# Optimization experiments

Measured on AMD Instinct MI355X. Metric: run time of the kernel, lower is better.

## Reference

```python
import jax, jax.numpy as jnp
import numpy as np
from jax import lax

# Surrogate spike: forward = Heaviside, backward = g / (1 + 5|x|)^2
@jax.custom_vjp
def spike_fn(x):
    return (x >= 0).astype(x.dtype)

def _spk_fwd(x):
    return spike_fn(x), x

def _spk_bwd(x, g):
    return (g / (1.0 + 5.0 * jnp.abs(x)) ** 2,)

spike_fn.defvjp(_spk_fwd, _spk_bwd)

BN_EPS = 1e-5

def _batchnorm(x, scale, bias, mean, var):
    # x: (B, C, T); eval-mode BN with running stats
    inv = scale / jnp.sqrt(var + BN_EPS)
    return x * inv[None, :, None] + (bias - mean * inv)[None, :, None]

def _conv1d(x, w, b, pad):
    y = lax.conv_general_dilated(x, w, (1,), [(pad, pad)],
                                 dimension_numbers=('NCH', 'OIH', 'NCH'))
    return y + b[None, :, None]

def setup_inputs() -> dict:
    key = jax.random.key(0)
    ks = jax.random.split(key, 12)
    B, T, EEG, GEO, TH, H, OUT = 4096, 320, 64, 18, 32, 16, 4
    inp = {
        'x_eeg': jax.random.normal(ks[0], (B, T, EEG), jnp.float32),
        'x_geo': jax.random.normal(ks[1], (B, T, GEO), jnp.float32),
        'conv1_w': jax.random.normal(ks[2], (TH, EEG, 5), jnp.float32) * 0.05,
        'conv1_b': jnp.zeros((TH,), jnp.float32),
        'bn1_s': jnp.ones((TH,), jnp.float32),
        'bn1_b': jnp.zeros((TH,), jnp.float32),
        'bn1_m': jnp.zeros((TH,), jnp.float32),
        'bn1_v': jnp.ones((TH,), jnp.float32),
        'conv2_w': jax.random.normal(ks[3], (H, TH, 3), jnp.float32) * 0.1,
        'conv2_b': jnp.zeros((H,), jnp.float32),
        'bn2_s': jnp.ones((H,), jnp.float32),
        'bn2_b': jnp.zeros((H,), jnp.float32),
        'bn2_m': jnp.zeros((H,), jnp.float32),
        'bn2_v': jnp.ones((H,), jnp.float32),
        'geo_w': jax.random.normal(ks[4], (H, GEO), jnp.float32) * 0.2,
        'geo_b': jnp.zeros((H,), jnp.float32),
        'gamma': jnp.full((H,), 0.5, jnp.float32),
        'fc1_w': jax.random.normal(ks[5], (64, 160), jnp.float32) * 0.08,
        'fc1_b': jnp.zeros((64,), jnp.float32),
        'fc2_w': jax.random.normal(ks[6], (OUT, 64), jnp.float32) * 0.12,
        'fc2_b': jnp.zeros((OUT,), jnp.float32),
    }
    return inp

def reference(x_eeg, x_geo, conv1_w, conv1_b, bn1_s, bn1_b, bn1_m, bn1_v,
              conv2_w, conv2_b, bn2_s, bn2_b, bn2_m, bn2_v,
              geo_w, geo_b, gamma, fc1_w, fc1_b, fc2_w, fc2_b):
    B, T, _ = x_eeg.shape
    theta_0, beta, tau_a, tau_m = 0.5, 1.8, 0.36, 0.8

    # EEG temporal encoder (eval mode: dropout = identity)
    h = x_eeg.transpose(0, 2, 1)  # (B, 64, T)
    h = jax.nn.relu(_batchnorm(_conv1d(h, conv1_w, conv1_b, 2), bn1_s, bn1_b, bn1_m, bn1_v))
    h = jax.nn.relu(_batchnorm(_conv1d(h, conv2_w, conv2_b, 1), bn2_s, bn2_b, bn2_m, bn2_v))
    eeg_encoded = h.transpose(0, 2, 1)  # (B, T, 16)

    geo_mod = jax.nn.sigmoid(jnp.einsum('bti,hi->bth', x_geo, geo_w) + geo_b)  # (B, T, 16)

    H = eeg_encoded.shape[-1]
    zeros = jnp.zeros((B, H), x_eeg.dtype)
    init = (zeros, zeros, zeros, zeros)  # mem_alif, eta, mem_li, prev_spk

    def step(carry, xs):
        mem_alif, eta, mem_li, prev_spk = carry
        cur_eeg, cur_geo = xs
        eta = tau_a * eta + (1.0 - tau_a) * prev_spk
        theta_t = theta_0 + beta * eta - gamma * cur_geo
        mem_alif = tau_m * mem_alif + cur_eeg
        spk = spike_fn(mem_alif - theta_t)
        mem_alif = mem_alif * (1.0 - spk)
        mem_li = 0.9 * mem_li + spk
        return (mem_alif, eta, mem_li, spk), mem_li

    xs = (eeg_encoded.transpose(1, 0, 2), geo_mod.transpose(1, 0, 2))  # (T, B, 16)
    _, pot = lax.scan(step, init, xs)  # (T, B, 16)

    pot = pot.transpose(1, 2, 0)                 # (B, 16, T)
    windows = pot.reshape(B, H, 10, 32)          # T = 320 = 10*32
    dp_feat = (windows[..., 16:].mean(-1) - windows[..., :16].mean(-1)).reshape(B, -1)  # (B, 160)

    out = jax.nn.relu(dp_feat @ fc1_w.T + fc1_b) @ fc2_w.T + fc2_b  # (B, 4)
    return out
```

## Files before the change

### kernel.cpp

```cpp
#include <hip/hip_runtime.h>
#include <math.h>

#define TB    4096
#define TSEQ  320
#define NEEG  64
#define NTH   32
#define NH    16
#define NGEO  18
#define TILE_T 64
#define NTILES 5
#define XROWS2 70
#define H1ROWS 66

typedef _Float16 f16x8 __attribute__((ext_vector_type(8)));
typedef _Float16 f16x2 __attribute__((ext_vector_type(2)));
typedef float f32x4 __attribute__((ext_vector_type(4)));
#define INV2048 4.8828125e-4f

#define OFF_W1F  0
#define OFF_W2F  10240
#define OFF_B1   11776
#define OFF_B2   11808
#define OFF_GWT  11824
#define OFF_FC1T 12112
#define OFF_FC2T 22352
#define OFF_ZP   22656
#define OFF_E    32768
#define SZ_EC    (TB*TSEQ*NH)
#define OFF_C    (OFF_E + SZ_EC)

__global__ void __launch_bounds__(256)
prep_kernel(const float* __restrict__ c1w, const float* __restrict__ c1b,
            const float* __restrict__ s1,  const float* __restrict__ bb1,
            const float* __restrict__ mm1, const float* __restrict__ vv1,
            const float* __restrict__ c2w, const float* __restrict__ c2b,
            const float* __restrict__ s2,  const float* __restrict__ bb2,
            const float* __restrict__ mm2, const float* __restrict__ vv2,
            const float* __restrict__ gw,  const float* __restrict__ fc1w,
            const float* __restrict__ fc2w, float* __restrict__ ws)
{
    const int tid = threadIdx.x;
    _Float16* w1fp = reinterpret_cast<_Float16*>(ws + OFF_W1F);
    _Float16* w2fp = reinterpret_cast<_Float16*>(ws + OFF_W2F);

    for (int d = tid; d < 10240; d += 256) {
        int j = d & 7, l = (d >> 3) & 63, nbk = d >> 9;
        int kk = nbk >> 1, nb = nbk & 1;
        int k = kk >> 1, i = (kk & 1) * 32 + ((l >> 4) * 8) + j;
        int c = nb * 16 + (l & 15);
        float inv = s1[c] / sqrtf(vv1[c] + 1e-5f);
        float wv = c1w[c * 320 + i * 5 + k] * inv;
        _Float16 hi = (_Float16)wv;
        _Float16 lo = (_Float16)((wv - (float)hi) * 2048.f);
        w1fp[((nbk * 2 + 0) * 64 + l) * 8 + j] = hi;
        w1fp[((nbk * 2 + 1) * 64 + l) * 8 + j] = lo;
    }
    for (int d = tid; d < 1536; d += 256) {
        int j = d & 7, l = (d >> 3) & 63, kk2 = d >> 9;
        int c = (l >> 4) * 8 + j;
        int o = l & 15;
        float inv = s2[o] / sqrtf(vv2[o] + 1e-5f);
        float wv = c2w[o * 96 + c * 3 + kk2] * inv;
        _Float16 hi = (_Float16)wv;
        _Float16 lo = (_Float16)((wv - (float)hi) * 2048.f);
        w2fp[((kk2 * 2 + 0) * 64 + l) * 8 + j] = hi;
        w2fp[((kk2 * 2 + 1) * 64 + l) * 8 + j] = lo;
    }
    if (tid < NTH) {
        float inv = s1[tid] / sqrtf(vv1[tid] + 1e-5f);
        ws[OFF_B1 + tid] = c1b[tid] * inv + bb1[tid] - mm1[tid] * inv;
    }
    if (tid < NH) {
        float inv = s2[tid] / sqrtf(vv2[tid] + 1e-5f);
        ws[OFF_B2 + tid] = c2b[tid] * inv + bb2[tid] - mm2[tid] * inv;
    }
    for (int d = tid; d < NGEO * NH; d += 256) {
        int i = d / NH, h = d - i * NH;
        ws[OFF_GWT + d] = gw[h * NGEO + i];
    }
    for (int d = tid; d < 160 * 64; d += 256) {
        int f = d / 64, o = d - f * 64;
        ws[OFF_FC1T + d] = fc1w[o * 160 + f];
    }
    if (tid < 256) {
        int j = tid / 4, o = tid - j * 4;
        ws[OFF_FC2T + tid] = fc2w[o * 64 + j];
    }
    if (tid < 64) ws[OFF_ZP + tid] = 0.f;
}

__global__ void __launch_bounds__(256, 2)
convm_kernel(const float* __restrict__ xeeg, const float* __restrict__ ws,
             float* __restrict__ E)
{
    __shared__ __align__(16) float xbuf[2][XROWS2 * 64];
    __shared__ __align__(16) _Float16 h1h[H1ROWS * 32];
    __shared__ __align__(16) _Float16 h1l[H1ROWS * 32];
    __shared__ float b1s[32], b2s[16];

    const int b = blockIdx.x, tid = threadIdx.x;
    const int l = tid & 63, w = tid >> 6;
    const int lrow = l & 15, lkg = l >> 4;
    const int nb = w >> 1, wsub = w & 1;

    const float* xb = xeeg + (size_t)b * TSEQ * NEEG;
    const float* zp = ws + OFF_ZP;

#define STAGE_DMA(buf, t0n) do {                                                     \
        for (int c_ = w; c_ < XROWS2; c_ += 4) {                                     \
            int tg_ = (t0n) - 3 + c_;                                                \
            const float* s_ = (tg_ >= 0 && tg_ < TSEQ)                               \
                              ? (xb + (size_t)tg_ * 64 + l) : zp;                    \
            __builtin_amdgcn_global_load_lds(                                        \
                (const __attribute__((address_space(1))) void*)s_,                   \
                (__attribute__((address_space(3))) void*)&xbuf[(buf)][c_ * 64],      \
                4, 0, 0);                                                            \
        }                                                                            \
    } while (0)

    f16x8 B1h[10], B1l[10], B2h[3], B2l[3];
    {
        const f16x8* wsrc = reinterpret_cast<const f16x8*>(ws + OFF_W1F);
        #pragma unroll
        for (int kk = 0; kk < 10; ++kk) {
            B1h[kk] = wsrc[((kk * 2 + nb) * 2 + 0) * 64 + l];
            B1l[kk] = wsrc[((kk * 2 + nb) * 2 + 1) * 64 + l];
        }
        const f16x8* wsrc2 = reinterpret_cast<const f16x8*>(ws + OFF_W2F);
        #pragma unroll
        for (int kk = 0; kk < 3; ++kk) {
            B2h[kk] = wsrc2[(kk * 2 + 0) * 64 + l];
            B2l[kk] = wsrc2[(kk * 2 + 1) * 64 + l];
        }
    }
    if (tid < 32) b1s[tid] = ws[OFF_B1 + tid];
    if (tid < 16) b2s[tid] = ws[OFF_B2 + tid];

    STAGE_DMA(0, 0);
    __syncthreads();

    for (int jt = 0; jt < NTILES; ++jt) {
        const int t0 = jt * TILE_T;
        const int cur = jt & 1;
        _Float16* xh = reinterpret_cast<_Float16*>(&xbuf[cur][0]);
        _Float16* xl = xh + XROWS2 * 64;

        float2 xr2[9];
        #pragma unroll
        for (int q = 0; q < 9; ++q) {
            int p = tid + q * 256;
            if (p < 2240) {
                int xr = p >> 5, ip = (p & 31) * 2;
                xr2[q] = *reinterpret_cast<const float2*>(&xbuf[cur][xr * 64 + ip]);
            }
        }
        __syncthreads();

        #pragma unroll
        for (int q = 0; q < 9; ++q) {
            int p = tid + q * 256;
            if (p < 2240) {
                int xr = p >> 5, ip = (p & 31) * 2;
                float f0 = xr2[q].x, f1 = xr2[q].y;
                _Float16 h0 = (_Float16)f0, h1v = (_Float16)f1;
                f16x2 vh = {h0, h1v};
                f16x2 vl = {(_Float16)((f0 - (float)h0) * 2048.f),
                            (_Float16)((f1 - (float)h1v) * 2048.f)};
                int idx = xr * 64 + (((ip >> 3) ^ (xr & 7)) << 3) + (ip & 7);
                *reinterpret_cast<f16x2*>(&xh[idx]) = vh;
                *reinterpret_cast<f16x2*>(&xl[idx]) = vl;
            }
        }
        __syncthreads();

        if (jt + 1 < NTILES) STAGE_DMA(cur ^ 1, (jt + 1) * TILE_T);
        __builtin_amdgcn_s_setprio(1);
        {
            const float bia = b1s[nb * 16 + lrow];
            #pragma unroll
            for (int pi = 0; pi < 3; ++pi) {
                if (pi == 2 && ((jt & 1) != wsub)) break;
                const int mb = (pi < 2) ? (wsub + pi * 2) : 4;
                const int mbase = mb * 16;
                int s = mbase + lrow; if (s > 65) s = 65;
                f32x4 aH = {0.f, 0.f, 0.f, 0.f};
                f32x4 aM = aH, aL = aH;
                #pragma unroll
                for (int kk = 0; kk < 10; ++kk) {
                    const int xr = s + (kk >> 1);
                    const int gx = (kk & 1) * 4 + lkg;
                    const int off = xr * 64 + ((gx ^ (xr & 7)) << 3);
                    f16x8 Ah = *reinterpret_cast<const f16x8*>(&xh[off]);
                    f16x8 Al = *reinterpret_cast<const f16x8*>(&xl[off]);
                    aH = __builtin_amdgcn_mfma_f32_16x16x32_f16(Ah, B1h[kk], aH, 0, 0, 0);
                    aM = __builtin_amdgcn_mfma_f32_16x16x32_f16(Ah, B1l[kk], aM, 0, 0, 0);
                    aL = __builtin_amdgcn_mfma_f32_16x16x32_f16(Al, B1h[kk], aL, 0, 0, 0);
                }
                #pragma unroll
                for (int r = 0; r < 4; ++r) {
                    int so = mbase + lkg * 4 + r;
                    if (so < 66) {
                        int tg = t0 - 1 + so;
                        bool v = (tg >= 0 && tg < TSEQ);
                        float val = v ? fmaxf(fmaf(aM[r] + aL[r], INV2048, aH[r]) + bia, 0.f) : 0.f;
                        int key = (so >> 1) & 3;
                        int g = (nb * 2 + (lrow >> 3)) ^ key;
                        int idx = so * 32 + (g << 3) + (lrow & 7);
                        _Float16 hh = (_Float16)val;
                        h1h[idx] = hh;
                        h1l[idx] = (_Float16)((val - (float)hh) * 2048.f);
                    }
                }
            }
        }
        __builtin_amdgcn_s_setprio(0);
        __syncthreads();

        {
            const int ub = w * 16;
            f32x4 aH = {0.f, 0.f, 0.f, 0.f};
            f32x4 aM = aH, aL = aH;
            __builtin_amdgcn_s_setprio(1);
            #pragma unroll
            for (int kk = 0; kk < 3; ++kk) {
                int srow = ub + lrow + kk;
                int off = srow * 32 + ((lkg ^ ((srow >> 1) & 3)) << 3);
                f16x8 Ah = *reinterpret_cast<const f16x8*>(&h1h[off]);
                f16x8 Al = *reinterpret_cast<const f16x8*>(&h1l[off]);
                aH = __builtin_amdgcn_mfma_f32_16x16x32_f16(Ah, B2h[kk], aH, 0, 0, 0);
                aM = __builtin_amdgcn_mfma_f32_16x16x32_f16(Ah, B2l[kk], aM, 0, 0, 0);
                aL = __builtin_amdgcn_mfma_f32_16x16x32_f16(Al, B2h[kk], aL, 0, 0, 0);
            }
            __builtin_amdgcn_s_setprio(0);
            const float bia = b2s[lrow];
            float4 ev;
            float* evp = reinterpret_cast<float*>(&ev);
            #pragma unroll
            for (int r = 0; r < 4; ++r)
                evp[r] = fmaxf(fmaf(aM[r] + aL[r], INV2048, aH[r]) + bia, 0.f);
            const int t4o = ((t0 + ub) >> 2) + lkg;
            float* ep = E + (((size_t)t4o * TB + b) * 16 + lrow) * 4;
            *reinterpret_cast<float4*>(ep) = ev;
        }
    }
#undef STAGE_DMA
}

__global__ void __launch_bounds__(256)
geo_kernel(const float* __restrict__ xgeo, const float* __restrict__ ws,
           const float* __restrict__ geo_b, const float* __restrict__ gamma,
           float* __restrict__ C)
{
    __shared__ float xgs[16][288];
    __shared__ float gws_l[NGEO * NH];
    __shared__ float gb_l[16], gam_l[16];

    const int tid = threadIdx.x;
    const int b0 = blockIdx.x * 16;
    const int s0 = blockIdx.y * 4;

    for (int p = tid; p < NGEO * NH; p += 256) gws_l[p] = ws[OFF_GWT + p];
    if (tid < 16) { gb_l[tid] = geo_b[tid]; gam_l[tid] = gamma[tid]; }
    {
        const float4* xg4 = reinterpret_cast<const float4*>(xgeo);
        for (int p = tid; p < 1152; p += 256) {
            int bb = p / 72, r = p - bb * 72;
            reinterpret_cast<float4*>(&xgs[bb][0])[r] =
                xg4[(size_t)(b0 + bb) * 1440 + (size_t)s0 * 18 + r];
        }
    }
    __syncthreads();

    const int h = tid & 15, bl = tid >> 4;
    #pragma unroll
    for (int k = 0; k < 4; ++k) {
        const int t4 = s0 + k;
        float4 cv;
        float* cvp = reinterpret_cast<float*>(&cv);
        #pragma unroll
        for (int tt = 0; tt < 4; ++tt) {
            float z = gb_l[h];
            const float* xr = &xgs[bl][(k * 4 + tt) * 18];
            #pragma unroll
            for (int ii = 0; ii < NGEO; ++ii)
                z = fmaf(xr[ii], gws_l[ii * 16 + h], z);
            cvp[tt] = gam_l[h] * (1.f / (1.f + expf(-z)));
        }
        float* cp = C + (((size_t)t4 * TB + (b0 + bl)) * 16 + h) * 4;
        *reinterpret_cast<float4*>(cp) = cv;
    }
}

__global__ void __launch_bounds__(256)
scanfc_kernel(const float* __restrict__ E, const float* __restrict__ C,
              const float* __restrict__ ws, const float* __restrict__ fc1_b,
              const float* __restrict__ fc2_b, float* __restrict__ out)
{
    __shared__ float dp_lds[16][160];
    __shared__ float mid[16][64];

    const int tid = threadIdx.x;
    const int h = tid & 15, bl = tid >> 4;
    const int b0 = blockIdx.x * 16;
    const int b = b0 + bl;

    const float4* e4 = reinterpret_cast<const float4*>(E);
    const float4* c4 = reinterpret_cast<const float4*>(C);
    const size_t slab = (size_t)TB * 16;
    const size_t idx = (size_t)b * 16 + h;

    float eta = 0.f, memv = 0.f, li = 0.f, ps = 0.f, accF = 0.f, accS = 0.f;

    float4 eA[4], cA[4], eB[4], cB[4];

#define LOADQ(EB, CB, lq) do {                                                   \
        if ((lq) < 20) {                                                         \
            _Pragma("unroll")                                                    \
            for (int j = 0; j < 4; ++j) {                                        \
                EB[j] = e4[(size_t)((lq) * 4 + j) * slab + idx];                 \
                CB[j] = c4[(size_t)((lq) * 4 + j) * slab + idx];                 \
            }                                                                    \
        }                                                                        \
    } while (0)

#define PROCQ(EB, CB, q) do {                                                    \
        _Pragma("unroll")                                                        \
        for (int j = 0; j < 4; ++j) {                                            \
            const int t4_ = (q) * 4 + j;                                         \
            const float* evp = reinterpret_cast<const float*>(&EB[j]);           \
            const float* cvp = reinterpret_cast<const float*>(&CB[j]);           \
            _Pragma("unroll")                                                    \
            for (int tt = 0; tt < 4; ++tt) {                                     \
                float e = evp[tt], c = cvp[tt];                                  \
                eta = 0.36f * eta + 0.64f * ps;                                  \
                float theta = 0.5f + 1.8f * eta - c;                             \
                memv = 0.8f * memv + e;                                          \
                float spk = (memv - theta >= 0.f) ? 1.f : 0.f;                   \
                memv *= (1.f - spk);                                             \
                li = 0.9f * li + spk;                                            \
                ps = spk;                                                        \
                int t = t4_ * 4 + tt;                                            \
                if (((t >> 4) & 1) == 0) accF += li; else accS += li;            \
            }                                                                    \
            if ((t4_ & 7) == 7) {                                                \
                dp_lds[bl][h * 10 + (t4_ >> 3)] = (accS - accF) * 0.0625f;       \
                accF = 0.f; accS = 0.f;                                          \
            }                                                                    \
        }                                                                        \
    } while (0)

    LOADQ(eA, cA, 0);
    for (int qp = 0; qp < 10; ++qp) {
        const int q0 = qp * 2, q1 = qp * 2 + 1;
        LOADQ(eB, cB, q1);
        PROCQ(eA, cA, q0);
        LOADQ(eA, cA, q1 + 1);
        PROCQ(eB, cB, q1);
    }
#undef LOADQ
#undef PROCQ
    __syncthreads();

    {
        const float* __restrict__ fc1t = ws + OFF_FC1T;
        #pragma unroll
        for (int k = 0; k < 4; ++k) {
            int id = tid + k * 256;
            int bb = id >> 6, o = id & 63;
            float z = fc1_b[o];
            for (int f = 0; f < 160; ++f)
                z = fmaf(dp_lds[bb][f], fc1t[f * 64 + o], z);
            mid[bb][o] = fmaxf(z, 0.f);
        }
    }
    __syncthreads();
    if (tid < 64) {
        const float* __restrict__ fc2t = ws + OFF_FC2T;
        int bb = tid >> 2, oo = tid & 3;
        float z = fc2_b[oo];
        #pragma unroll
        for (int jj = 0; jj < 64; ++jj)
            z = fmaf(mid[bb][jj], fc2t[jj * 4 + oo], z);
        out[(size_t)(b0 + bb) * 4 + oo] = z;
    }
}

extern "C" void kernel_launch(void* const* d_in, const int* in_sizes, int n_in,
                              void* d_out, int out_size, void* d_ws, size_t ws_size,
                              hipStream_t stream)
{
    const float* xeeg = (const float*)d_in[0];
    const float* xgeo = (const float*)d_in[1];
    const float* c1w  = (const float*)d_in[2];
    const float* c1b  = (const float*)d_in[3];
    const float* s1   = (const float*)d_in[4];
    const float* bb1  = (const float*)d_in[5];
    const float* mm1  = (const float*)d_in[6];
    const float* vv1  = (const float*)d_in[7];
    const float* c2w  = (const float*)d_in[8];
    const float* c2b  = (const float*)d_in[9];
    const float* s2   = (const float*)d_in[10];
    const float* bb2  = (const float*)d_in[11];
    const float* mm2  = (const float*)d_in[12];
    const float* vv2  = (const float*)d_in[13];
    const float* gw   = (const float*)d_in[14];
    const float* gb   = (const float*)d_in[15];
    const float* gam  = (const float*)d_in[16];
    const float* fc1w = (const float*)d_in[17];
    const float* fc1b = (const float*)d_in[18];
    const float* fc2w = (const float*)d_in[19];
    const float* fc2b = (const float*)d_in[20];
    float* ws   = (float*)d_ws;
    float* outp = (float*)d_out;

    hipLaunchKernelGGL(prep_kernel, dim3(1), dim3(256), 0, stream,
                       c1w, c1b, s1, bb1, mm1, vv1, c2w, c2b, s2, bb2, mm2, vv2,
                       gw, fc1w, fc2w, ws);

    float* E = ws + OFF_E;
    float* C = ws + OFF_C;
    hipLaunchKernelGGL(geo_kernel, dim3(TB / 16, TSEQ / 16), dim3(256), 0, stream,
                       xgeo, ws, gb, gam, C);
    hipLaunchKernelGGL(convm_kernel, dim3(TB), dim3(256), 0, stream,
                       xeeg, ws, E);
    hipLaunchKernelGGL(scanfc_kernel, dim3(TB / 16), dim3(256), 0, stream,
                       E, C, ws, fc1b, fc2b, outp);
}
```

Measured before the change: 300.7 us.

## Fuse geo modulation into scan kernel with double-buffered LDS staging of x_geo

Removes the separate geo_kernel and its intermediate C buffer (TB*T*16 floats written then read back). The scan kernel now stages x_geo tiles into a double-buffered shared array and computes the sigmoid-gated geo term inline per timestep. This saves the global round-trip of C and one kernel launch. In exchange it adds per-step FMA and exp work inside the serial scan and block-wide syncs, while the scan kernel only has 256 blocks.

```diff
diff --git a/kernel.cpp b/kernel.cpp
--- a/kernel.cpp
+++ b/kernel.cpp
@@ -27,7 +27,6 @@
 #define OFF_ZP   22656
 #define OFF_E    32768
 #define SZ_EC    (TB*TSEQ*NH)
-#define OFF_C    (OFF_E + SZ_EC)
 
 __global__ void __launch_bounds__(256)
 prep_kernel(const float* __restrict__ c1w, const float* __restrict__ c1b,
@@ -247,55 +246,14 @@
 }
 
 __global__ void __launch_bounds__(256)
-geo_kernel(const float* __restrict__ xgeo, const float* __restrict__ ws,
-           const float* __restrict__ geo_b, const float* __restrict__ gamma,
-           float* __restrict__ C)
+scanfc_kernel(const float* __restrict__ E, const float* __restrict__ xgeo,
+              const float* __restrict__ ws, const float* __restrict__ geo_b,
+              const float* __restrict__ gamma, const float* __restrict__ fc1_b,
+              const float* __restrict__ fc2_b, float* __restrict__ out)
 {
-    __shared__ float xgs[16][288];
+    __shared__ float xgs[2][16][288];
     __shared__ float gws_l[NGEO * NH];
     __shared__ float gb_l[16], gam_l[16];
-
-    const int tid = threadIdx.x;
-    const int b0 = blockIdx.x * 16;
-    const int s0 = blockIdx.y * 4;
-
-    for (int p = tid; p < NGEO * NH; p += 256) gws_l[p] = ws[OFF_GWT + p];
-    if (tid < 16) { gb_l[tid] = geo_b[tid]; gam_l[tid] = gamma[tid]; }
-    {
-        const float4* xg4 = reinterpret_cast<const float4*>(xgeo);
-        for (int p = tid; p < 1152; p += 256) {
-            int bb = p / 72, r = p - bb * 72;
-            reinterpret_cast<float4*>(&xgs[bb][0])[r] =
-                xg4[(size_t)(b0 + bb) * 1440 + (size_t)s0 * 18 + r];
-        }
-    }
-    __syncthreads();
-
-    const int h = tid & 15, bl = tid >> 4;
-    #pragma unroll
-    for (int k = 0; k < 4; ++k) {
-        const int t4 = s0 + k;
-        float4 cv;
-        float* cvp = reinterpret_cast<float*>(&cv);
-        #pragma unroll
-        for (int tt = 0; tt < 4; ++tt) {
-            float z = gb_l[h];
-            const float* xr = &xgs[bl][(k * 4 + tt) * 18];
-            #pragma unroll
-            for (int ii = 0; ii < NGEO; ++ii)
-                z = fmaf(xr[ii], gws_l[ii * 16 + h], z);
-            cvp[tt] = gam_l[h] * (1.f / (1.f + expf(-z)));
-        }
-        float* cp = C + (((size_t)t4 * TB + (b0 + bl)) * 16 + h) * 4;
-        *reinterpret_cast<float4*>(cp) = cv;
-    }
-}
-
-__global__ void __launch_bounds__(256)
-scanfc_kernel(const float* __restrict__ E, const float* __restrict__ C,
-              const float* __restrict__ ws, const float* __restrict__ fc1_b,
-              const float* __restrict__ fc2_b, float* __restrict__ out)
-{
     __shared__ float dp_lds[16][160];
     __shared__ float mid[16][64];
 
@@ -304,34 +262,47 @@
     const int b0 = blockIdx.x * 16;
     const int b = b0 + bl;
 
-    const float4* e4 = reinterpret_cast<const float4*>(E);
-    const float4* c4 = reinterpret_cast<const float4*>(C);
+    const float4* e4  = reinterpret_cast<const float4*>(E);
+    const float4* xg4 = reinterpret_cast<const float4*>(xgeo);
     const size_t slab = (size_t)TB * 16;
     const size_t idx = (size_t)b * 16 + h;
 
+    for (int p = tid; p < NGEO * NH; p += 256) gws_l[p] = ws[OFF_GWT + p];
+    if (tid < 16) { gb_l[tid] = geo_b[tid]; gam_l[tid] = gamma[tid]; }
+
     float eta = 0.f, memv = 0.f, li = 0.f, ps = 0.f, accF = 0.f, accS = 0.f;
-
-    float4 eA[4], cA[4], eB[4], cB[4];
-
-#define LOADQ(EB, CB, lq) do {                                                   \
+    float4 eA[4], eB[4];
+
+#define STAGE_XG(buf, q) do {                                                    \
+        for (int p = tid; p < 1152; p += 256) {                                  \
+            int bb = p / 72, r = p - bb * 72;                                    \
+            reinterpret_cast<float4*>(&xgs[buf][bb][0])[r] =                     \
+                xg4[(size_t)(b0 + bb) * 1440 + (size_t)(q) * 72 + r];            \
+        }                                                                        \
+    } while (0)
+
+#define LOADQ(EB, lq) do {                                                       \
         if ((lq) < 20) {                                                         \
             _Pragma("unroll")                                                    \
-            for (int j = 0; j < 4; ++j) {                                        \
+            for (int j = 0; j < 4; ++j)                                          \
                 EB[j] = e4[(size_t)((lq) * 4 + j) * slab + idx];                 \
-                CB[j] = c4[(size_t)((lq) * 4 + j) * slab + idx];                 \
-            }                                                                    \
         }                                                                        \
     } while (0)
 
-#define PROCQ(EB, CB, q) do {                                                    \
+#define PROCQG(EB, XP, q) do {                                                   \
         _Pragma("unroll")                                                        \
         for (int j = 0; j < 4; ++j) {                                            \
             const int t4_ = (q) * 4 + j;                                         \
             const float* evp = reinterpret_cast<const float*>(&EB[j]);           \
-            const float* cvp = reinterpret_cast<const float*>(&CB[j]);           \
             _Pragma("unroll")                                                    \
             for (int tt = 0; tt < 4; ++tt) {                                     \
-                float e = evp[tt], c = cvp[tt];                                  \
+                const float* xr_ = &XP[bl][(j * 4 + tt) * 18];                   \
+                float z = gb_l[h];                                               \
+                _Pragma("unroll")                                                \
+                for (int ii = 0; ii < 18; ++ii)                                  \
+                    z = fmaf(xr_[ii], gws_l[ii * 16 + h], z);                    \
+                float c = gam_l[h] * (1.f / (1.f + expf(-z)));                   \
+                float e = evp[tt];                                               \
                 eta = 0.36f * eta + 0.64f * ps;                                  \
                 float theta = 0.5f + 1.8f * eta - c;                             \
                 memv = 0.8f * memv + e;                                          \
@@ -349,16 +320,24 @@
         }                                                                        \
     } while (0)
 
-    LOADQ(eA, cA, 0);
+    STAGE_XG(0, 0);
+    LOADQ(eA, 0);
+    __syncthreads();
+
     for (int qp = 0; qp < 10; ++qp) {
         const int q0 = qp * 2, q1 = qp * 2 + 1;
-        LOADQ(eB, cB, q1);
-        PROCQ(eA, cA, q0);
-        LOADQ(eA, cA, q1 + 1);
-        PROCQ(eB, cB, q1);
-    }
+        if (q0 < 19) STAGE_XG(1, q0 + 1);
+        LOADQ(eB, q1);
+        PROCQG(eA, xgs[0], q0);
+        __syncthreads();
+        if (q1 < 19) STAGE_XG(0, q1 + 1);
+        LOADQ(eA, q1 + 1);
+        PROCQG(eB, xgs[1], q1);
+        if (qp < 9) __syncthreads();
+    }
+#undef STAGE_XG
 #undef LOADQ
-#undef PROCQ
+#undef PROCQG
     __syncthreads();
 
     {
@@ -418,11 +397,8 @@
                        gw, fc1w, fc2w, ws);
 
     float* E = ws + OFF_E;
-    float* C = ws + OFF_C;
-    hipLaunchKernelGGL(geo_kernel, dim3(TB / 16, TSEQ / 16), dim3(256), 0, stream,
-                       xgeo, ws, gb, gam, C);
     hipLaunchKernelGGL(convm_kernel, dim3(TB), dim3(256), 0, stream,
                        xeeg, ws, E);
     hipLaunchKernelGGL(scanfc_kernel, dim3(TB / 16), dim3(256), 0, stream,
-                       E, C, ws, fc1b, fc2b, outp);
+                       E, xgeo, ws, gb, gam, fc1b, fc2b, outp);
 }
```

Measured after the change: 321.0 us. 1.07x slower.
